# Kernel optimization log

Hardware: AMD Instinct MI355X
Metric: run time of the kernel (lower is better)

Reference implementation:

```python
import jax, jax.numpy as jnp
import numpy as np

IGNORE_INDEX = -100


def setup_inputs() -> dict:
    key = jax.random.key(0)
    k1, k2, k3 = jax.random.split(key, 3)
    B, S, D, V = 2, 4096, 2048, 32000
    outputs = jax.random.normal(k1, (B, S, D), dtype=jnp.float32)
    # LM-head weight, nn.Linear convention: [vocab, embed_dim], scaled like typical init
    weight = jax.random.normal(k2, (V, D), dtype=jnp.float32) * (D ** -0.5)
    targets = jax.random.randint(k3, (B, S), 0, V, dtype=jnp.int64)
    return {"outputs": outputs, "weight": weight, "targets": targets}


def reference(outputs, weight, targets):
    # Flatten tokens: [B, S, D] -> [N, D], [B, S] -> [N]
    D = outputs.shape[-1]
    x = outputs.reshape(-1, D)            # [N, D]
    t = targets.reshape(-1)               # [N]
    # Fused linear projection: logits [N, V]
    logits = jnp.einsum("nd,vd->nv", x, weight)
    logp = jax.nn.log_softmax(logits, axis=-1)
    valid = t != IGNORE_INDEX
    safe_t = jnp.where(valid, t, 0)
    # Gather target log-prob per token
    nll = -jnp.take_along_axis(logp, safe_t[:, None], axis=1)[:, 0]  # [N]
    n_valid = jnp.maximum(jnp.sum(valid.astype(nll.dtype)), 1.0)
    loss = jnp.sum(jnp.where(valid, nll, 0.0)) / n_valid
    return loss
```

## Files before the change

### kernel.cpp

```cpp
#include <hip/hip_runtime.h>
#include <hip/hip_bf16.h>
#include <math.h>

#define IGNORE_INDEX (-100)

typedef __attribute__((ext_vector_type(4))) float f32x4;
typedef __attribute__((ext_vector_type(16))) float f32x16;
typedef __attribute__((ext_vector_type(4))) int i32x4;
typedef __attribute__((ext_vector_type(8))) int i32x8;

static const int NTOK = 2 * 4096;
static const int DIM  = 2048;
static const int VOC  = 32000;
static const int BM = 128, BN = 128;
static const int KS = 64;
static const int NPH = DIM / KS;
static const int NVT = VOC / BN;
static const int MT  = NTOK / BM;
static const float WSCALE = 16.0f;
#define SCL1 0x7F7F7F7F


__device__ inline void gload_lds16(const void* g, void* l) {
  __builtin_amdgcn_global_load_lds(
      (const __attribute__((address_space(1))) void*)g,
      (__attribute__((address_space(3))) void*)l,
      16, 0, 0);
}


__global__ void cast_f32_fp8(const float* __restrict__ in,
                             unsigned char* __restrict__ out, long n8, float scale) {
  long i0 = (long)blockIdx.x * blockDim.x + threadIdx.x;
  long stride = (long)gridDim.x * blockDim.x;
  for (long i = i0; i < n8; i += stride) {
    const float4* p = (const float4*)(in + i * 8);
    float4 a = p[0], b = p[1];
    int lo = __builtin_amdgcn_cvt_pk_fp8_f32(a.x * scale, a.y * scale, 0, false);
    lo = __builtin_amdgcn_cvt_pk_fp8_f32(a.z * scale, a.w * scale, lo, true);
    int hi = __builtin_amdgcn_cvt_pk_fp8_f32(b.x * scale, b.y * scale, 0, false);
    hi = __builtin_amdgcn_cvt_pk_fp8_f32(b.z * scale, b.w * scale, hi, true);
    int2 o; o.x = lo; o.y = hi;
    *(int2*)(out + i * 8) = o;
  }
}


#define VM0  asm volatile("s_waitcnt vmcnt(0)" ::: "memory")
#define BARRIER asm volatile("s_barrier" ::: "memory")

#define MS(ACC, AV, BV) \
  ACC = __builtin_amdgcn_mfma_scale_f32_32x32x64_f8f6f4( \
      AV, BV, ACC, 0, 0, 0, SCL1, 0, SCL1)

#define PACK8(LO, HI) {LO[0], LO[1], LO[2], LO[3], HI[0], HI[1], HI[2], HI[3]}

#define STAGE(DST) do { \
  char* _dA = stA + (DST) * 8192; \
  char* _dB = stB + (DST) * 8192; \
  gload_lds16(aS0, _dA); \
  gload_lds16(aS1, _dA + 1024); \
  gload_lds16(bS0, _dB); \
  gload_lds16(bS1, _dB + 1024); \
  aS0 += KS; aS1 += KS; bS0 += KS; bS1 += KS; \
} while (0)

#define SLOT_COMPUTE(RING) do { \
  const char* _Ab = aRd + (RING) * 8192; \
  const char* _Bb = bRd + (RING) * 8192; \
  i32x4 qb0l = *(const i32x4*)(_Bb);        i32x4 qb0h = *(const i32x4*)(_Bb + 1024); \
  i32x4 qa0l = *(const i32x4*)(_Ab);        i32x4 qa0h = *(const i32x4*)(_Ab + 1024); \
  i32x4 qb1l = *(const i32x4*)(_Bb + 2048); i32x4 qb1h = *(const i32x4*)(_Bb + 3072); \
  i32x4 qa1l = *(const i32x4*)(_Ab + 2048); i32x4 qa1h = *(const i32x4*)(_Ab + 3072); \
  i32x8 _B0 = PACK8(qb0l, qb0h); \
  i32x8 _A0 = PACK8(qa0l, qa0h); \
  i32x8 _B1 = PACK8(qb1l, qb1h); \
  i32x8 _A1 = PACK8(qa1l, qa1h); \
  __builtin_amdgcn_s_setprio(1); \
  MS(acc[0][0], _A0, _B0); MS(acc[0][1], _A0, _B1); \
  MS(acc[1][0], _A1, _B0); MS(acc[1][1], _A1, _B1); \
  __builtin_amdgcn_s_setprio(0); \
} while (0)

__launch_bounds__(256, 4)
__global__ void lce_gemm(const unsigned char* __restrict__ xq,
                         const unsigned char* __restrict__ wq,
                         float* __restrict__ pmax, float* __restrict__ psum) {
  extern __shared__ char smem[];
  char* smA = smem;
  char* smB = smem + 16384;

  const int nwg = NVT * MT;
  const int cpx = nwg >> 3;
  const int bid = blockIdx.x;
  const int swz = (bid & 7) * cpx + (bid >> 3);
  const int vt = swz / MT;
  const int mt = swz % MT;
  const int m0 = mt * BM;
  const int v0 = vt * BN;

  const int tid = threadIdx.x;
  const int lane = tid & 63;
  const int w = tid >> 6;
  const int wr = w >> 1, wc = w & 1;
  const int lc = lane & 31;
  const int lh = lane >> 5;

  f32x16 acc[2][2];
#pragma unroll
  for (int i = 0; i < 2; ++i)
#pragma unroll
    for (int j = 0; j < 2; ++j)
#pragma unroll
      for (int r = 0; r < 16; ++r) acc[i][j][r] = 0.f;

  const unsigned char* aS0 = xq + (long)(m0 + w * 32 + lc) * DIM + lh * 32;
  const unsigned char* aS1 = aS0 + 16;
  const unsigned char* bS0 = wq + (long)(v0 + w * 32 + lc) * DIM + lh * 32;
  const unsigned char* bS1 = bS0 + 16;
  char* stA = smA + w * 2048;
  char* stB = smB + w * 2048;

  const char* aRd = smA + wr * 4096 + lane * 16;
  const char* bRd = smB + wc * 4096 + lane * 16;

  STAGE(0);

#pragma unroll 1
  for (int n = 0; n < NPH; ++n) {
    VM0;
    BARRIER;
    if (n < NPH - 1) STAGE((n + 1) & 1);
    SLOT_COMPUTE(n & 1);
  }

  const float sc = 1.0f / WSCALE;
  float* sm_m = (float*)smem;
  float* sm_s = (float*)(smem + 1024);
  __syncthreads();
#pragma unroll
  for (int i = 0; i < 2; ++i) {
#pragma unroll
    for (int r = 0; r < 16; ++r) {
      float l0 = acc[i][0][r] * sc, l1 = acc[i][1][r] * sc;
      float m = fmaxf(l0, l1);
#pragma unroll
      for (int mk = 1; mk < 32; mk <<= 1) m = fmaxf(m, __shfl_xor(m, mk));
      float s = __expf(l0 - m) + __expf(l1 - m);
#pragma unroll
      for (int mk = 1; mk < 32; mk <<= 1) s += __shfl_xor(s, mk);
      if (lc == 0) {
        int R = wr * 64 + i * 32 + (r & 3) + 8 * (r >> 2) + 4 * lh;
        sm_m[wc * 128 + R] = m;
        sm_s[wc * 128 + R] = s;
      }
    }
  }
  __syncthreads();
  if (tid < BM) {
    float ma = sm_m[tid], mb = sm_m[128 + tid];
    float gm = fmaxf(ma, mb);
    float gs = sm_s[tid] * __expf(ma - gm) + sm_s[128 + tid] * __expf(mb - gm);
    long row = (long)(m0 + tid);
    pmax[row * NVT + vt] = gm;
    psum[row * NVT + vt] = gs;
  }
}


__global__ void token_reduce(const float* __restrict__ x, const float* __restrict__ wgt,
                             const int* __restrict__ tgt,
                             const float* __restrict__ pmax, const float* __restrict__ psum,
                             float* __restrict__ nll, float* __restrict__ validf) {
  const int n = blockIdx.x;
  const int tid = threadIdx.x;
  const int lane = tid & 63;
  const int w = tid >> 6;
  __shared__ float smr[4];

  const int t = tgt[n];
  const bool valid = (t != IGNORE_INDEX);
  const int ts = valid ? t : 0;

  const float4* xr = (const float4*)(x + (long)n * DIM);
  const float4* wr = (const float4*)(wgt + (long)ts * DIM);
  float d = 0.f;
  for (int i = tid; i < DIM / 4; i += blockDim.x) {
    float4 a = xr[i], b = wr[i];
    d += a.x * b.x + a.y * b.y + a.z * b.z + a.w * b.w;
  }

  float m = (tid < NVT) ? pmax[(long)n * NVT + tid] : -INFINITY;
  float t1 = m;
#pragma unroll
  for (int mk = 1; mk < 64; mk <<= 1) t1 = fmaxf(t1, __shfl_xor(t1, mk));
  if (lane == 0) smr[w] = t1;
  __syncthreads();
  const float gm = fmaxf(fmaxf(smr[0], smr[1]), fmaxf(smr[2], smr[3]));
  __syncthreads();

  float se = (tid < NVT) ? psum[(long)n * NVT + tid] * __expf(m - gm) : 0.f;
#pragma unroll
  for (int mk = 1; mk < 64; mk <<= 1) se += __shfl_xor(se, mk);
  if (lane == 0) smr[w] = se;
  __syncthreads();
  const float gs = smr[0] + smr[1] + smr[2] + smr[3];
  __syncthreads();

#pragma unroll
  for (int mk = 1; mk < 64; mk <<= 1) d += __shfl_xor(d, mk);
  if (lane == 0) smr[w] = d;
  __syncthreads();
  const float gd = smr[0] + smr[1] + smr[2] + smr[3];

  if (tid == 0) {
    nll[n] = valid ? (gm + logf(gs) - gd) : 0.f;
    validf[n] = valid ? 1.f : 0.f;
  }
}


__global__ void final_reduce(const float* __restrict__ nll, const float* __restrict__ validf,
                             float* __restrict__ out, int n) {
  const int tid = threadIdx.x;
  const int lane = tid & 63;
  const int w = tid >> 6;
  __shared__ float sm1[4], sm2[4];
  float s = 0.f, c = 0.f;
  for (int i = tid; i < n; i += blockDim.x) { s += nll[i]; c += validf[i]; }
#pragma unroll
  for (int mk = 1; mk < 64; mk <<= 1) { s += __shfl_xor(s, mk); c += __shfl_xor(c, mk); }
  if (lane == 0) { sm1[w] = s; sm2[w] = c; }
  __syncthreads();
  if (tid == 0) {
    float ts = sm1[0] + sm1[1] + sm1[2] + sm1[3];
    float tc = sm2[0] + sm2[1] + sm2[2] + sm2[3];
    out[0] = ts / fmaxf(tc, 1.0f);
  }
}


extern "C" void kernel_launch(void* const* d_in, const int* in_sizes, int n_in,
                              void* d_out, int out_size, void* d_ws, size_t ws_size,
                              hipStream_t stream) {
  const float* x = (const float*)d_in[0];
  const float* wgt = (const float*)d_in[1];
  const int* tgt = (const int*)d_in[2];
  float* out = (float*)d_out;

  char* ws = (char*)d_ws;
  const size_t xq_off = 0;
  const size_t wq_off = (size_t)NTOK * DIM;
  const size_t pm_off = wq_off + (size_t)VOC * DIM;
  const size_t ps_off = pm_off + (size_t)NTOK * NVT * 4;
  const size_t nl_off = ps_off + (size_t)NTOK * NVT * 4;
  const size_t vf_off = nl_off + (size_t)NTOK * 4;
  const size_t needed = vf_off + (size_t)NTOK * 4;
  if (ws_size < needed) return;

  unsigned char* xq = (unsigned char*)(ws + xq_off);
  unsigned char* wq = (unsigned char*)(ws + wq_off);
  float* pmax = (float*)(ws + pm_off);
  float* psum = (float*)(ws + ps_off);
  float* nllv = (float*)(ws + nl_off);
  float* vldf = (float*)(ws + vf_off);

  cast_f32_fp8<<<2048, 256, 0, stream>>>(x, xq, (long)NTOK * DIM / 8, 1.0f);
  cast_f32_fp8<<<4096, 256, 0, stream>>>(wgt, wq, (long)VOC * DIM / 8, WSCALE);

  (void)hipFuncSetAttribute((const void*)lce_gemm,
                            hipFuncAttributeMaxDynamicSharedMemorySize, 32768);
  lce_gemm<<<NVT * MT, 256, 32768, stream>>>(xq, wq, pmax, psum);

  token_reduce<<<NTOK, 256, 0, stream>>>(x, wgt, tgt, pmax, psum, nllv, vldf);
  final_reduce<<<1, 256, 0, stream>>>(nllv, vldf, out, NTOK);
}
```

Before: 1.106 ms.

## Switch GEMM to 16x16x128 FP8 MFMA with single-buffered K=128 tiles

Replaces the 32x32x64 scaled MFMA with the 16x16x128 variant, giving each wave a 4x4 grid of 16x16 accumulators and a K step of 128 bytes per iteration. It drops the double-buffered async staging pipeline in favour of a load, syncthreads, compute loop with static shared memory. The softmax epilogue is rewritten for the 16-lane row layout. The change halves the number of K iterations but loses overlap between global-to-LDS loads and MFMA work, and it removes the occupancy hint from the launch bounds.

New measurement: 1.032 ms. 1.07x faster.

```diff
diff --git a/kernel.cpp b/kernel.cpp
--- a/kernel.cpp
+++ b/kernel.cpp
@@ -5,7 +5,6 @@
 #define IGNORE_INDEX (-100)
 
 typedef __attribute__((ext_vector_type(4))) float f32x4;
-typedef __attribute__((ext_vector_type(16))) float f32x16;
 typedef __attribute__((ext_vector_type(4))) int i32x4;
 typedef __attribute__((ext_vector_type(8))) int i32x8;
 
@@ -13,8 +12,8 @@
 static const int DIM  = 2048;
 static const int VOC  = 32000;
 static const int BM = 128, BN = 128;
-static const int KS = 64;
-static const int NPH = DIM / KS;
+static const int BKB = 128;
+static const int NKS = DIM / BKB;
 static const int NVT = VOC / BN;
 static const int MT  = NTOK / BM;
 static const float WSCALE = 16.0f;
@@ -46,49 +45,18 @@
 }
 
 
-#define VM0  asm volatile("s_waitcnt vmcnt(0)" ::: "memory")
-#define BARRIER asm volatile("s_barrier" ::: "memory")
-
-#define MS(ACC, AV, BV) \
-  ACC = __builtin_amdgcn_mfma_scale_f32_32x32x64_f8f6f4( \
+#define MS4(ACC, AV, BV) \
+  ACC = __builtin_amdgcn_mfma_scale_f32_16x16x128_f8f6f4( \
       AV, BV, ACC, 0, 0, 0, SCL1, 0, SCL1)
 
 #define PACK8(LO, HI) {LO[0], LO[1], LO[2], LO[3], HI[0], HI[1], HI[2], HI[3]}
 
-#define STAGE(DST) do { \
-  char* _dA = stA + (DST) * 8192; \
-  char* _dB = stB + (DST) * 8192; \
-  gload_lds16(aS0, _dA); \
-  gload_lds16(aS1, _dA + 1024); \
-  gload_lds16(bS0, _dB); \
-  gload_lds16(bS1, _dB + 1024); \
-  aS0 += KS; aS1 += KS; bS0 += KS; bS1 += KS; \
-} while (0)
-
-#define SLOT_COMPUTE(RING) do { \
-  const char* _Ab = aRd + (RING) * 8192; \
-  const char* _Bb = bRd + (RING) * 8192; \
-  i32x4 qb0l = *(const i32x4*)(_Bb);        i32x4 qb0h = *(const i32x4*)(_Bb + 1024); \
-  i32x4 qa0l = *(const i32x4*)(_Ab);        i32x4 qa0h = *(const i32x4*)(_Ab + 1024); \
-  i32x4 qb1l = *(const i32x4*)(_Bb + 2048); i32x4 qb1h = *(const i32x4*)(_Bb + 3072); \
-  i32x4 qa1l = *(const i32x4*)(_Ab + 2048); i32x4 qa1h = *(const i32x4*)(_Ab + 3072); \
-  i32x8 _B0 = PACK8(qb0l, qb0h); \
-  i32x8 _A0 = PACK8(qa0l, qa0h); \
-  i32x8 _B1 = PACK8(qb1l, qb1h); \
-  i32x8 _A1 = PACK8(qa1l, qa1h); \
-  __builtin_amdgcn_s_setprio(1); \
-  MS(acc[0][0], _A0, _B0); MS(acc[0][1], _A0, _B1); \
-  MS(acc[1][0], _A1, _B0); MS(acc[1][1], _A1, _B1); \
-  __builtin_amdgcn_s_setprio(0); \
-} while (0)
-
-__launch_bounds__(256, 4)
+__launch_bounds__(256)
 __global__ void lce_gemm(const unsigned char* __restrict__ xq,
                          const unsigned char* __restrict__ wq,
                          float* __restrict__ pmax, float* __restrict__ psum) {
-  extern __shared__ char smem[];
-  char* smA = smem;
-  char* smB = smem + 16384;
+  __shared__ __align__(16) char smA[16384];
+  __shared__ __align__(16) char smB[16384];
 
   const int nwg = NVT * MT;
   const int cpx = nwg >> 3;
@@ -103,54 +71,83 @@
   const int lane = tid & 63;
   const int w = tid >> 6;
   const int wr = w >> 1, wc = w & 1;
-  const int lc = lane & 31;
-  const int lh = lane >> 5;
-
-  f32x16 acc[2][2];
-#pragma unroll
-  for (int i = 0; i < 2; ++i)
-#pragma unroll
-    for (int j = 0; j < 2; ++j)
-#pragma unroll
-      for (int r = 0; r < 16; ++r) acc[i][j][r] = 0.f;
-
-  const unsigned char* aS0 = xq + (long)(m0 + w * 32 + lc) * DIM + lh * 32;
-  const unsigned char* aS1 = aS0 + 16;
-  const unsigned char* bS0 = wq + (long)(v0 + w * 32 + lc) * DIM + lh * 32;
-  const unsigned char* bS1 = bS0 + 16;
-  char* stA = smA + w * 2048;
-  char* stB = smB + w * 2048;
-
-  const char* aRd = smA + wr * 4096 + lane * 16;
-  const char* bRd = smB + wc * 4096 + lane * 16;
-
-  STAGE(0);
+  const int li = lane & 15, lg = lane >> 4;
+
+  f32x4 acc[4][4];
+  const f32x4 z = {0.f, 0.f, 0.f, 0.f};
+#pragma unroll
+  for (int i = 0; i < 4; ++i)
+#pragma unroll
+    for (int j = 0; j < 4; ++j) acc[i][j] = z;
+
+  const unsigned char* aP0 = xq + (long)(m0 + 2 * w * 16 + li) * DIM + lg * 32;
+  const unsigned char* aP1 = xq + (long)(m0 + (2 * w + 1) * 16 + li) * DIM + lg * 32;
+  const unsigned char* bP0 = wq + (long)(v0 + 2 * w * 16 + li) * DIM + lg * 32;
+  const unsigned char* bP1 = wq + (long)(v0 + (2 * w + 1) * 16 + li) * DIM + lg * 32;
+  char* dA0 = smA + 2 * w * 2048;
+  char* dA1 = smA + (2 * w + 1) * 2048;
+  char* dB0 = smB + 2 * w * 2048;
+  char* dB1 = smB + (2 * w + 1) * 2048;
+
+  const char* aRd = smA + wr * 4 * 2048 + lane * 16;
+  const char* bRd = smB + wc * 4 * 2048 + lane * 16;
 
 #pragma unroll 1
-  for (int n = 0; n < NPH; ++n) {
-    VM0;
-    BARRIER;
-    if (n < NPH - 1) STAGE((n + 1) & 1);
-    SLOT_COMPUTE(n & 1);
+  for (int ks = 0; ks < NKS; ++ks) {
+    __syncthreads();
+    gload_lds16(aP0, dA0);      gload_lds16(aP0 + 16, dA0 + 1024);
+    gload_lds16(aP1, dA1);      gload_lds16(aP1 + 16, dA1 + 1024);
+    gload_lds16(bP0, dB0);      gload_lds16(bP0 + 16, dB0 + 1024);
+    gload_lds16(bP1, dB1);      gload_lds16(bP1 + 16, dB1 + 1024);
+    aP0 += BKB; aP1 += BKB; bP0 += BKB; bP1 += BKB;
+    __syncthreads();
+
+    i32x4 a0l = *(const i32x4*)(aRd);        i32x4 a0h = *(const i32x4*)(aRd + 1024);
+    i32x4 a1l = *(const i32x4*)(aRd + 2048); i32x4 a1h = *(const i32x4*)(aRd + 3072);
+    i32x4 a2l = *(const i32x4*)(aRd + 4096); i32x4 a2h = *(const i32x4*)(aRd + 5120);
+    i32x4 a3l = *(const i32x4*)(aRd + 6144); i32x4 a3h = *(const i32x4*)(aRd + 7168);
+    i32x4 b0l = *(const i32x4*)(bRd);        i32x4 b0h = *(const i32x4*)(bRd + 1024);
+    i32x4 b1l = *(const i32x4*)(bRd + 2048); i32x4 b1h = *(const i32x4*)(bRd + 3072);
+    i32x4 b2l = *(const i32x4*)(bRd + 4096); i32x4 b2h = *(const i32x4*)(bRd + 5120);
+    i32x4 b3l = *(const i32x4*)(bRd + 6144); i32x4 b3h = *(const i32x4*)(bRd + 7168);
+
+    i32x8 A0 = PACK8(a0l, a0h);
+    i32x8 A1 = PACK8(a1l, a1h);
+    i32x8 A2 = PACK8(a2l, a2h);
+    i32x8 A3 = PACK8(a3l, a3h);
+    i32x8 B0 = PACK8(b0l, b0h);
+    i32x8 B1 = PACK8(b1l, b1h);
+    i32x8 B2 = PACK8(b2l, b2h);
+    i32x8 B3 = PACK8(b3l, b3h);
+
+    MS4(acc[0][0], A0, B0); MS4(acc[0][1], A0, B1);
+    MS4(acc[0][2], A0, B2); MS4(acc[0][3], A0, B3);
+    MS4(acc[1][0], A1, B0); MS4(acc[1][1], A1, B1);
+    MS4(acc[1][2], A1, B2); MS4(acc[1][3], A1, B3);
+    MS4(acc[2][0], A2, B0); MS4(acc[2][1], A2, B1);
+    MS4(acc[2][2], A2, B2); MS4(acc[2][3], A2, B3);
+    MS4(acc[3][0], A3, B0); MS4(acc[3][1], A3, B1);
+    MS4(acc[3][2], A3, B2); MS4(acc[3][3], A3, B3);
   }
 
   const float sc = 1.0f / WSCALE;
-  float* sm_m = (float*)smem;
-  float* sm_s = (float*)(smem + 1024);
-  __syncthreads();
-#pragma unroll
-  for (int i = 0; i < 2; ++i) {
-#pragma unroll
-    for (int r = 0; r < 16; ++r) {
+  float* sm_m = (float*)smA;
+  float* sm_s = (float*)(smA + 2048);
+  __syncthreads();
+#pragma unroll
+  for (int i = 0; i < 4; ++i) {
+#pragma unroll
+    for (int r = 0; r < 4; ++r) {
       float l0 = acc[i][0][r] * sc, l1 = acc[i][1][r] * sc;
-      float m = fmaxf(l0, l1);
-#pragma unroll
-      for (int mk = 1; mk < 32; mk <<= 1) m = fmaxf(m, __shfl_xor(m, mk));
-      float s = __expf(l0 - m) + __expf(l1 - m);
-#pragma unroll
-      for (int mk = 1; mk < 32; mk <<= 1) s += __shfl_xor(s, mk);
-      if (lc == 0) {
-        int R = wr * 64 + i * 32 + (r & 3) + 8 * (r >> 2) + 4 * lh;
+      float l2 = acc[i][2][r] * sc, l3 = acc[i][3][r] * sc;
+      float m = fmaxf(fmaxf(l0, l1), fmaxf(l2, l3));
+#pragma unroll
+      for (int mk = 1; mk < 16; mk <<= 1) m = fmaxf(m, __shfl_xor(m, mk));
+      float s = __expf(l0 - m) + __expf(l1 - m) + __expf(l2 - m) + __expf(l3 - m);
+#pragma unroll
+      for (int mk = 1; mk < 16; mk <<= 1) s += __shfl_xor(s, mk);
+      if (li == 0) {
+        int R = wr * 64 + i * 16 + lg * 4 + r;
         sm_m[wc * 128 + R] = m;
         sm_s[wc * 128 + R] = s;
       }
@@ -268,9 +265,7 @@
   cast_f32_fp8<<<2048, 256, 0, stream>>>(x, xq, (long)NTOK * DIM / 8, 1.0f);
   cast_f32_fp8<<<4096, 256, 0, stream>>>(wgt, wq, (long)VOC * DIM / 8, WSCALE);
 
-  (void)hipFuncSetAttribute((const void*)lce_gemm,
-                            hipFuncAttributeMaxDynamicSharedMemorySize, 32768);
-  lce_gemm<<<NVT * MT, 256, 32768, stream>>>(xq, wq, pmax, psum);
+  lce_gemm<<<NVT * MT, 256, 0, stream>>>(xq, wq, pmax, psum);
 
   token_reduce<<<NTOK, 256, 0, stream>>>(x, wgt, tgt, pmax, psum, nllv, vldf);
   final_reduce<<<1, 256, 0, stream>>>(nllv, vldf, out, NTOK);
```
